# Optimization experiments

Measured on AMD Instinct MI355X. Metric: run time of the kernel, lower is better.

Reference implementation:

```python
import jax, jax.numpy as jnp
import numpy as np

L, CIN, CKV, E, H, D, NQ, NK = 3, 128, 256, 128, 8, 16, 4096, 1024
CLAMP_MAX = 65503.0  # torch.clamp(max=65503)
SCALE = 1.0 / (D * D)  # non-standard: 1 / projection_dim**2


def group_norm(x, w, b, groups, eps=1e-5):
    # x: [..., C, N]; w, b broadcastable to x.shape[:-1] (i.e. lead + (C,))
    lead = x.shape[:-2]
    C, N = x.shape[-2:]
    xg = x.reshape(lead + (groups, C // groups, N))
    mu = xg.mean(axis=(-2, -1), keepdims=True)
    var = ((xg - mu) ** 2).mean(axis=(-2, -1), keepdims=True)
    xn = ((xg - mu) * jax.lax.rsqrt(var + eps)).reshape(lead + (C, N))
    return xn * w[..., None] + b[..., None]


def split_heads(t):
    # [L, 1, E, N] -> [L, 1, H, N, D]
    l, b, e, n = t.shape
    return t.transpose(0, 1, 3, 2).reshape(l, b, n, H, D).transpose(0, 1, 3, 2, 4)


def setup_inputs():
    key = jax.random.key(0)
    ks = jax.random.split(key, 18)
    r = lambda k, s: jax.random.normal(k, s, dtype=jnp.float32)
    return {
        'x': r(ks[0], (1, CIN, NQ)),
        'x_global': r(ks[1], (L, CKV, NK)),
        'xyz': r(ks[2], (1, NQ, 3)),
        'xyz_global': r(ks[3], (L, NK, 3)),
        'gn1_w': r(ks[4], (CIN,)), 'gn1_b': r(ks[5], (CIN,)),
        'gn2_w': r(ks[6], (L, CKV)), 'gn2_b': r(ks[7], (L, CKV)),
        'qw': r(ks[8], (L, E, CIN)) * 0.05, 'qb': r(ks[9], (L, E)),
        'kw': r(ks[10], (L, E, CKV)) * 0.05, 'kb': r(ks[11], (L, E)),
        'vw': r(ks[12], (L, E, CKV)) * 0.05, 'vb': r(ks[13], (L, E)),
        'qgn_w': r(ks[14], (L, E)), 'qgn_b': r(ks[15], (L, E)),
        'cw': r(ks[16], (L, CIN, E)) * 0.05, 'cb': r(ks[17], (L, CIN)),
    }


def reference(x, x_global, xyz, xyz_global, gn1_w, gn1_b, gn2_w, gn2_b,
              qw, qb, kw, kb, vw, vb, qgn_w, qgn_b, cw, cb):
    # pre-norm of query features (shared across layers): [1, CIN, NQ]
    xq = jax.nn.relu(group_norm(x, gn1_w, gn1_b, 8))
    # per-source KV features: [L, 1, CKV, NK]
    xg = jax.nn.relu(group_norm(x_global[:, None], gn2_w[:, None], gn2_b[:, None], 16))

    # conv1d (kernel=1) projections + the shared q_gn GroupNorm(8, E)
    q = jnp.einsum('lec,bcn->lben', qw, xq) + qb[:, None, :, None]        # [L,1,E,NQ]
    q = group_norm(q, qgn_w[:, None], qgn_b[:, None], 8)
    k = jnp.einsum('lec,lbcn->lben', kw, xg) + kb[:, None, :, None]       # [L,1,E,NK]
    k = group_norm(k, qgn_w[:, None], qgn_b[:, None], 8)
    v = jnp.einsum('lec,lbcn->lben', vw, xg) + vb[:, None, :, None]       # [L,1,E,NK]
    v = group_norm(v, qgn_w[:, None], qgn_b[:, None], 8)

    qh, kh, vh = split_heads(q), split_heads(k), split_heads(v)           # [L,1,H,*,D]

    score = jnp.einsum('lbhqd,lbhkd->lbhqk', qh * SCALE, kh)              # [L,1,H,NQ,NK]
    score = jnp.minimum(score, CLAMP_MAX)
    w_att = jax.nn.softmax(score, axis=-1)
    o = jnp.einsum('lbhqk,lbhkd->lbhqd', w_att, vh)                        # [L,1,H,NQ,D]
    o = o.transpose(0, 1, 3, 2, 4).reshape(L, 1, NQ, E)                    # merge heads
    o = jnp.einsum('lbqe,loe->lbqo', o, cw) + cb[:, None, None, :]         # combine heads
    o = o.transpose(0, 1, 3, 2) + xq[None]                                 # [L,1,CIN,NQ], SA residual

    out = o.mean(axis=0) + x                                               # mean over sources + block residual
    return out, w_att[-1]                                                  # weight of last layer, as in torch loop
```

## Files before the change

### kernel.cpp

```cpp
#include <hip/hip_runtime.h>
#include <math.h>

constexpr int NQ = 4096, NK = 1024, CIN = 128, CKV = 256, E = 128, H = 8, D = 16, LAYERS = 3;
constexpr float SCALE = 1.0f / 256.0f;
constexpr float LOG2E = 1.44269504088896340736f;

typedef __bf16 bf16x8 __attribute__((ext_vector_type(8)));
typedef __bf16 bf16x4 __attribute__((ext_vector_type(4)));
typedef float f32x16 __attribute__((ext_vector_type(16)));
typedef float f32x4 __attribute__((ext_vector_type(4)));

__device__ __forceinline__ float exp2_fast(float x) {
#if __has_builtin(__builtin_amdgcn_exp2f)
  return __builtin_amdgcn_exp2f(x);
#else
  return exp2f(x);
#endif
}

__device__ __forceinline__ float rcp_fast(float x) {
#if __has_builtin(__builtin_amdgcn_rcpf)
  return __builtin_amdgcn_rcpf(x);
#else
  return 1.f / x;
#endif
}

__device__ __forceinline__ void block_reduce2(float& a, float& b, float* red) {
#pragma unroll
  for (int off = 32; off > 0; off >>= 1) {
    a += __shfl_down(a, off, 64);
    b += __shfl_down(b, off, 64);
  }
  int lane = threadIdx.x & 63, wid = threadIdx.x >> 6;
  if (lane == 0) { red[wid * 2] = a; red[wid * 2 + 1] = b; }
  __syncthreads();
  if (threadIdx.x == 0) {
    float sa = 0.f, sb = 0.f;
#pragma unroll
    for (int w = 0; w < 4; w++) { sa += red[w * 2]; sb += red[w * 2 + 1]; }
    red[0] = sa; red[1] = sb;
  }
  __syncthreads();
  a = red[0]; b = red[1];
}

__global__ __launch_bounds__(256) void pre_partial(const float* __restrict__ x,
                                                   const float* __restrict__ xg,
                                                   const float* __restrict__ qw,
                                                   const float* __restrict__ kw,
                                                   const float* __restrict__ vw,
                                                   float* __restrict__ acc,
                                                   __bf16* __restrict__ qwb,
                                                   __bf16* __restrict__ kwb,
                                                   __bf16* __restrict__ vwb) {
  int b = blockIdx.x, t = threadIdx.x;
  if (b >= 640) {
    int i = b - 640;
    const float* src; __bf16* dst; int off;
    if (i < 24)      { src = qw; dst = qwb; off = i * 2048; }
    else if (i < 72) { src = kw; dst = kwb; off = (i - 24) * 2048; }
    else             { src = vw; dst = vwb; off = (i - 72) * 2048; }
    int base = off + t * 8;
    float4 a = *(const float4*)(src + base);
    float4 c = *(const float4*)(src + base + 4);
    bf16x8 o = { (__bf16)a.x, (__bf16)a.y, (__bf16)a.z, (__bf16)a.w,
                 (__bf16)c.x, (__bf16)c.y, (__bf16)c.z, (__bf16)c.w };
    *(bf16x8*)(dst + base) = o;
    return;
  }
  __shared__ float red[8];
  const float4* p;
  int aidx;
  if (b < 256) { p = (const float4*)x + (size_t)b * 512; aidx = b >> 5; }
  else { int i = b - 256; p = (const float4*)xg + (size_t)i * 512; aidx = 8 + (i >> 3); }
  float s = 0.f, sq = 0.f;
#pragma unroll
  for (int i = 0; i < 2; i++) {
    float4 v = p[t + i * 256];
    s += v.x + v.y + v.z + v.w;
    sq += v.x * v.x + v.y * v.y + v.z * v.z + v.w * v.w;
  }
  block_reduce2(s, sq, red);
  if (t == 0) {
    atomicAdd(&acc[aidx * 2], s);
    atomicAdd(&acc[aidx * 2 + 1], sq);
  }
}

__global__ __launch_bounds__(256) void stage_a(const float* __restrict__ x,
                                               const float* __restrict__ xg,
                                               const float* __restrict__ acc,
                                               const float* __restrict__ gn1w,
                                               const float* __restrict__ gn1b,
                                               const float* __restrict__ gn2w,
                                               const float* __restrict__ gn2b,
                                               __bf16* __restrict__ xq_t,
                                               __bf16* __restrict__ xg_t) {
  int b = blockIdx.x, t = threadIdx.x;
  __shared__ float T[128 * 36];
  const float* in; __bf16* out; int N, Cout, ccbase, n0, gbase;
  const float* gw; const float* gb; float inv;
  if (b < 128) {
    in = x; N = NQ; out = xq_t; Cout = 128; ccbase = 0; n0 = b * 32;
    gw = gn1w; gb = gn1b; gbase = 0; inv = 1.f / 65536.f;
  } else {
    int i = b - 128; int l = i / 64; int r = i % 64; int ch = r >> 5;
    n0 = (r & 31) * 32;
    in = xg + ((size_t)l * 256 + ch * 128) * 1024; N = NK;
    out = xg_t + (size_t)l * 1024 * 256; Cout = 256; ccbase = ch * 128;
    gw = gn2w + l * 256 + ch * 128; gb = gn2b + l * 256 + ch * 128;
    gbase = 8 + l * 16 + ch * 8; inv = 1.f / 16384.f;
  }
  int nq = t & 7, cbase = t >> 3;
#pragma unroll
  for (int i = 0; i < 4; i++) {
    int c = cbase + 32 * i;
    int g = gbase + (c >> 4);
    float mu = acc[2 * g] * inv;
    float rs = rsqrtf(acc[2 * g + 1] * inv - mu * mu + 1e-5f);
    float sc = gw[c] * rs, sh = gb[c] - mu * sc;
    float4 v = *(const float4*)(in + (size_t)c * N + n0 + nq * 4);
    float4 o;
    o.x = fmaxf(v.x * sc + sh, 0.f);
    o.y = fmaxf(v.y * sc + sh, 0.f);
    o.z = fmaxf(v.z * sc + sh, 0.f);
    o.w = fmaxf(v.w * sc + sh, 0.f);
    *(float4*)(T + c * 36 + nq * 4) = o;
  }
  __syncthreads();
  int n = t >> 3, c0 = (t & 7) * 16;
  bf16x8 o1, o2;
#pragma unroll
  for (int j = 0; j < 8; j++) {
    o1[j] = (__bf16)T[(c0 + j) * 36 + n];
    o2[j] = (__bf16)T[(c0 + 8 + j) * 36 + n];
  }
  __bf16* op = out + (size_t)(n0 + n) * Cout + ccbase + c0;
  *(bf16x8*)op = o1;
  *(bf16x8*)(op + 8) = o2;
}

template <int KSTEPS>
__device__ __forceinline__ void gemm_tile(const __bf16* __restrict__ A,
                                          const __bf16* __restrict__ Bm,
                                          int stride, f32x16& acc, int l31, int half) {
#pragma unroll
  for (int ks = 0; ks < KSTEPS; ks++) {
    bf16x8 af = *(const bf16x8*)(A + (size_t)l31 * stride + ks * 16 + half * 8);
    bf16x8 bf = *(const bf16x8*)(Bm + (size_t)l31 * stride + ks * 16 + half * 8);
    acc = __builtin_amdgcn_mfma_f32_32x32x16_bf16(af, bf, acc, 0, 0, 0);
  }
}

__global__ __launch_bounds__(256) void proj_mfma(const __bf16* __restrict__ xq_t,
                                                 const __bf16* __restrict__ xg_t,
                                                 const __bf16* __restrict__ qwb,
                                                 const __bf16* __restrict__ kwb,
                                                 const __bf16* __restrict__ vwb,
                                                 const float* __restrict__ qb,
                                                 const float* __restrict__ kb,
                                                 const float* __restrict__ vb,
                                                 __bf16* __restrict__ q_raw,
                                                 __bf16* __restrict__ k_raw,
                                                 __bf16* __restrict__ v_raw,
                                                 float* __restrict__ qgnAcc) {
  int t = threadIdx.x;
  int w = blockIdx.x * 4 + (t >> 6);
  int lane = t & 63, l31 = lane & 31, half = lane >> 5;
  f32x16 acc = {0.f,0.f,0.f,0.f,0.f,0.f,0.f,0.f,0.f,0.f,0.f,0.f,0.f,0.f,0.f,0.f};
  int mat, l, e0, n0, N;
  const __bf16* A; const __bf16* Bm; const float* bias;
  if (w < 1536) {
    mat = 0; l = w >> 9; int r = w & 511; e0 = (r & 3) * 32; n0 = (r >> 2) * 32;
    N = NQ; A = qwb + (size_t)l * 128 * 128; Bm = xq_t; bias = qb + l * 128;
  } else if (w < 1920) {
    mat = 1; int idx = w - 1536; l = idx >> 7; int r = idx & 127;
    e0 = (r & 3) * 32; n0 = (r >> 2) * 32;
    N = NK; A = kwb + (size_t)l * 128 * 256; Bm = xg_t + (size_t)l * 1024 * 256;
    bias = kb + l * 128;
  } else {
    mat = 2; int idx = w - 1920; l = idx >> 7; int r = idx & 127;
    e0 = (r & 3) * 32; n0 = (r >> 2) * 32;
    N = NK; A = vwb + (size_t)l * 128 * 256; Bm = xg_t + (size_t)l * 1024 * 256;
    bias = vb + l * 128;
  }
  if (mat == 0) {
    gemm_tile<8>(A + (size_t)e0 * 128, Bm + (size_t)n0 * 128, 128, acc, l31, half);
  } else {
    gemm_tile<16>(A + (size_t)e0 * 256, Bm + (size_t)n0 * 256, 256, acc, l31, half);
  }

  float vals[16];
  float s0 = 0.f, sq0 = 0.f, s1 = 0.f, sq1 = 0.f;
#pragma unroll
  for (int r = 0; r < 16; r++) {
    int row = (r & 3) + 8 * (r >> 2) + 4 * half;
    float v = acc[r] + bias[e0 + row];
    vals[r] = v;
    if (r < 8) { s0 += v; sq0 += v * v; } else { s1 += v; sq1 += v * v; }
  }
#pragma unroll
  for (int off = 1; off < 64; off <<= 1) {
    s0 += __shfl_xor(s0, off); sq0 += __shfl_xor(sq0, off);
    s1 += __shfl_xor(s1, off); sq1 += __shfl_xor(sq1, off);
  }
  int gbase = (mat == 0 ? 0 : (mat == 1 ? 24 : 48)) + l * 8 + (e0 >> 4);
  if (lane == 0) {
    atomicAdd(&qgnAcc[gbase * 2], s0);
    atomicAdd(&qgnAcc[gbase * 2 + 1], sq0);
    atomicAdd(&qgnAcc[(gbase + 1) * 2], s1);
    atomicAdd(&qgnAcc[(gbase + 1) * 2 + 1], sq1);
  }
  if (mat < 2) {
    __bf16* out = (mat == 0 ? q_raw : k_raw);
#pragma unroll
    for (int qd = 0; qd < 4; qd++) {
      int h = (e0 >> 4) + (qd >> 1);
      int d0 = 4 * half + 8 * (qd & 1);
      bf16x4 o;
#pragma unroll
      for (int j = 0; j < 4; j++) o[j] = (__bf16)vals[qd * 4 + j];
      *(bf16x4*)(out + ((size_t)(l * 8 + h) * N + n0 + l31) * 16 + d0) = o;
    }
  } else {
#pragma unroll
    for (int r = 0; r < 16; r++) {
      int row = (r & 3) + 8 * (r >> 2) + 4 * half;
      int h = (e0 >> 4) + (row >> 4);
      v_raw[((size_t)(l * 8 + h) * 16 + (row & 15)) * NK + n0 + l31] = (__bf16)vals[r];
    }
  }
}

__global__ __launch_bounds__(256) void attn_kernel(const __bf16* __restrict__ qbf,
                                                   const __bf16* __restrict__ kbf,
                                                   const __bf16* __restrict__ vbf,
                                                   const float* __restrict__ qgnAcc,
                                                   const float* __restrict__ qgnw,
                                                   const float* __restrict__ qgnb,
                                                   float* __restrict__ ob,
                                                   float* __restrict__ rinv_ws) {
  __shared__ __bf16 Pt[4][32 * 40];

  const int t = threadIdx.x;
  const int wv = t >> 6;
  const int lane = t & 63;
  const int l31 = lane & 31, half = lane >> 5, l15 = lane & 15, quad = lane >> 4;
  const int h = blockIdx.y, l = blockIdx.z;
  const int q0 = blockIdx.x * 128 + wv * 32;

  const __bf16* Qh = qbf + (size_t)(l * H + h) * NQ * D;
  const __bf16* Kh = kbf + (size_t)(l * H + h) * NK * D;
  const __bf16* Vh = vbf + (size_t)(l * H + h) * D * NK;

  const int gq = l * 8 + h, gk = 24 + l * 8 + h, gv = 48 + l * 8 + h;
  const float invq = 1.f / 65536.f, invkv = 1.f / 16384.f;
  const float muq = qgnAcc[2 * gq] * invq;
  const float rsq = rsqrtf(qgnAcc[2 * gq + 1] * invq - muq * muq + 1e-5f);
  const float muk = qgnAcc[2 * gk] * invkv;
  const float rsk = rsqrtf(qgnAcc[2 * gk + 1] * invkv - muk * muk + 1e-5f);
  const float muv = qgnAcc[2 * gv] * invkv;
  const float rsv = rsqrtf(qgnAcc[2 * gv + 1] * invkv - muv * muv + 1e-5f);

  const int cbase = l * 128 + h * 16;
  bf16x8 qfrag;
  {
    const float EX = SCALE * LOG2E;
    bf16x8 qraw = *(const bf16x8*)(Qh + (size_t)(q0 + l31) * D + half * 8);
#pragma unroll
    for (int j = 0; j < 8; j++) {
      float w = qgnw[cbase + half * 8 + j], bb = qgnb[cbase + half * 8 + j];
      float wq = w * rsq;
      float qe = (float)qraw[j] * (wq * EX) + (bb - muq * wq) * EX;
      qfrag[j] = (__bf16)(qe * (w * rsk));
    }
  }
  const float va = qgnw[cbase + l15] * rsv;
  const float vc = qgnb[cbase + l15] - muv * va;

  bf16x8 ones;
#pragma unroll
  for (int j = 0; j < 8; j++) ones[j] = (__bf16)1.0f;

  f32x4 oa0 = {0.f, 0.f, 0.f, 0.f}, oa1 = {0.f, 0.f, 0.f, 0.f};
  f32x4 sa0 = {0.f, 0.f, 0.f, 0.f}, sa1 = {0.f, 0.f, 0.f, 0.f};

  __bf16* Pw = &Pt[wv][0];

  for (int c = 0; c < 32; ++c) {
    const int k0 = c * 32;
    bf16x8 kf = *(const bf16x8*)(Kh + (size_t)(k0 + l31) * D + half * 8);
    f32x16 s = {0.f,0.f,0.f,0.f,0.f,0.f,0.f,0.f,0.f,0.f,0.f,0.f,0.f,0.f,0.f,0.f};
    s = __builtin_amdgcn_mfma_f32_32x32x16_bf16(qfrag, kf, s, 0, 0, 0);
#pragma unroll
    for (int r = 0; r < 16; ++r) {
      float p = exp2_fast(s[r]);
      int row = (r & 3) + 8 * (r >> 2) + 4 * half;
      Pw[row * 40 + l31] = (__bf16)p;
    }
    bf16x8 a0 = *(const bf16x8*)(Pw + l15 * 40 + quad * 8);
    bf16x8 a1 = *(const bf16x8*)(Pw + (16 + l15) * 40 + quad * 8);
    bf16x8 bv = *(const bf16x8*)(Vh + (size_t)l15 * NK + k0 + quad * 8);
    oa0 = __builtin_amdgcn_mfma_f32_16x16x32_bf16(a0, bv, oa0, 0, 0, 0);
    oa1 = __builtin_amdgcn_mfma_f32_16x16x32_bf16(a1, bv, oa1, 0, 0, 0);
    sa0 = __builtin_amdgcn_mfma_f32_16x16x32_bf16(a0, ones, sa0, 0, 0, 0);
    sa1 = __builtin_amdgcn_mfma_f32_16x16x32_bf16(a1, ones, sa1, 0, 0, 0);
  }

  if (l == 2 && l15 == 0) {
#pragma unroll
    for (int r = 0; r < 4; ++r) {
      rinv_ws[(size_t)h * NQ + q0 + quad * 4 + r] = rcp_fast(sa0[r]);
      rinv_ws[(size_t)h * NQ + q0 + 16 + quad * 4 + r] = rcp_fast(sa1[r]);
    }
  }

  float* Ow = (float*)Pw;
#pragma unroll
  for (int r = 0; r < 4; ++r) {
    int qa = quad * 4 + r;
    Ow[l15 * 36 + qa] = oa0[r] * rcp_fast(sa0[r]) * va + vc;
    Ow[l15 * 36 + 16 + qa] = oa1[r] * rcp_fast(sa1[r]) * va + vc;
  }
  {
    int dd = lane >> 2, j = (lane & 3) * 8;
    float4 u0 = *(const float4*)(Ow + dd * 36 + j);
    float4 u1 = *(const float4*)(Ow + dd * 36 + j + 4);
    size_t rb = (size_t)(l * E + h * D + dd) * NQ + q0 + j;
    *(float4*)(ob + rb) = u0;
    *(float4*)(ob + rb + 4) = u1;
  }
}

__global__ __launch_bounds__(256) void post_kernel(const __bf16* __restrict__ qbf,
                                                   const __bf16* __restrict__ kbf,
                                                   const float* __restrict__ rinv_ws,
                                                   const float* __restrict__ qgnAcc,
                                                   const float* __restrict__ qgnw,
                                                   const float* __restrict__ qgnb,
                                                   const float* __restrict__ x,
                                                   const float* __restrict__ accAll,
                                                   const float* __restrict__ gn1w,
                                                   const float* __restrict__ gn1b,
                                                   const float* __restrict__ ob,
                                                   const float* __restrict__ cw,
                                                   const float* __restrict__ cb,
                                                   float* __restrict__ out,
                                                   float* __restrict__ wout) {
  __shared__ float S[128 * 16];
  const int blk = blockIdx.x, t = threadIdx.x;
  if (blk < 512) {
    const int wv = t >> 6, lane = t & 63;
    const int l31 = lane & 31, half = lane >> 5;
    const int qtile = blk & 31, h = (blk >> 5) & 7, khalf = blk >> 8;
    const int q0 = qtile * 128 + wv * 32;
    const int kbase = khalf * 512;

    const __bf16* Qh = qbf + (size_t)(2 * H + h) * NQ * D;
    const __bf16* Kh = kbf + (size_t)(2 * H + h) * NK * D;

    const int gq = 16 + h, gk = 24 + 16 + h;
    const float invq = 1.f / 65536.f, invkv = 1.f / 16384.f;
    const float muq = qgnAcc[2 * gq] * invq;
    const float rsq = rsqrtf(qgnAcc[2 * gq + 1] * invq - muq * muq + 1e-5f);
    const float muk = qgnAcc[2 * gk] * invkv;
    const float rsk = rsqrtf(qgnAcc[2 * gk + 1] * invkv - muk * muk + 1e-5f);

    const int cbase = 2 * 128 + h * 16;
    bf16x8 qfrag;
    {
      const float EX = SCALE * LOG2E;
      bf16x8 qraw = *(const bf16x8*)(Qh + (size_t)(q0 + l31) * D + half * 8);
#pragma unroll
      for (int j = 0; j < 8; j++) {
        float w = qgnw[cbase + half * 8 + j], bb = qgnb[cbase + half * 8 + j];
        float wq = w * rsq;
        float qe = (float)qraw[j] * (wq * EX) + (bb - muq * wq) * EX;
        qfrag[j] = (__bf16)(qe * (w * rsk));
      }
    }

    float riv[16];
#pragma unroll
    for (int r = 0; r < 16; ++r)
      riv[r] = rinv_ws[(size_t)h * NQ + q0 + (r & 3) + 8 * (r >> 2) + 4 * half];

    for (int c = 0; c < 16; ++c) {
      const int k0 = kbase + c * 32;
      bf16x8 kf = *(const bf16x8*)(Kh + (size_t)(k0 + l31) * D + half * 8);
      f32x16 s = {0.f,0.f,0.f,0.f,0.f,0.f,0.f,0.f,0.f,0.f,0.f,0.f,0.f,0.f,0.f,0.f};
      s = __builtin_amdgcn_mfma_f32_32x32x16_bf16(qfrag, kf, s, 0, 0, 0);
#pragma unroll
      for (int r = 0; r < 16; ++r) {
        float p = exp2_fast(s[r]) * riv[r];
        int row = (r & 3) + 8 * (r >> 2) + 4 * half;
        __builtin_nontemporal_store(p, &wout[(size_t)(h * NQ + q0 + row) * NK + k0 + l31]);
      }
    }
    return;
  }

  const int nt0 = (blk - 512) * 16;
  const int c0 = (t >> 2) * 2;
  const int nf = t & 3;
  float4 a0 = make_float4(0.f, 0.f, 0.f, 0.f);
  float4 a1 = make_float4(0.f, 0.f, 0.f, 0.f);
  for (int l = 0; l < LAYERS; l++) {
    if (l) __syncthreads();
#pragma unroll
    for (int i = 0; i < 2; i++) {
      int fid = i * 256 + t;
      int e = fid >> 2, pos = fid & 3;
      *(float4*)(S + e * 16 + pos * 4) =
          *(const float4*)(ob + ((size_t)l * E + e) * NQ + nt0 + pos * 4);
    }
    __syncthreads();
    const float* cwl = cw + (size_t)l * CIN * E;
#pragma unroll 8
    for (int e4 = 0; e4 < E / 4; e4++) {
      const int e = e4 * 4;
      float4 w0 = *(const float4*)(cwl + (size_t)c0 * E + e);
      float4 w1 = *(const float4*)(cwl + (size_t)(c0 + 1) * E + e);
      float4 s0 = *(const float4*)(S + (e + 0) * 16 + nf * 4);
      float4 s1 = *(const float4*)(S + (e + 1) * 16 + nf * 4);
      float4 s2 = *(const float4*)(S + (e + 2) * 16 + nf * 4);
      float4 s3 = *(const float4*)(S + (e + 3) * 16 + nf * 4);
      a0.x += w0.x * s0.x + w0.y * s1.x + w0.z * s2.x + w0.w * s3.x;
      a0.y += w0.x * s0.y + w0.y * s1.y + w0.z * s2.y + w0.w * s3.y;
      a0.z += w0.x * s0.z + w0.y * s1.z + w0.z * s2.z + w0.w * s3.z;
      a0.w += w0.x * s0.w + w0.y * s1.w + w0.z * s2.w + w0.w * s3.w;
      a1.x += w1.x * s0.x + w1.y * s1.x + w1.z * s2.x + w1.w * s3.x;
      a1.y += w1.x * s0.y + w1.y * s1.y + w1.z * s2.y + w1.w * s3.y;
      a1.z += w1.x * s0.z + w1.y * s1.z + w1.z * s2.z + w1.w * s3.z;
      a1.w += w1.x * s0.w + w1.y * s1.w + w1.z * s2.w + w1.w * s3.w;
    }
  }
  const float third = 1.f / 3.f;
#pragma unroll
  for (int i = 0; i < 2; i++) {
    int c = c0 + i;
    float4 a = i ? a1 : a0;
    float bsum = (cb[c] + cb[CIN + c] + cb[2 * CIN + c]) * third;
    int g = c >> 4;
    const float inv = 1.f / 65536.f;
    float mu = accAll[2 * g] * inv;
    float rs = rsqrtf(accAll[2 * g + 1] * inv - mu * mu + 1e-5f);
    float sc = gn1w[c] * rs, sh = gn1b[c] - mu * sc;
    size_t off = (size_t)c * NQ + nt0 + nf * 4;
    float4 xv = *(const float4*)(x + off);
    float4 o;
    o.x = xv.x + fmaxf(xv.x * sc + sh, 0.f) + a.x * third + bsum;
    o.y = xv.y + fmaxf(xv.y * sc + sh, 0.f) + a.y * third + bsum;
    o.z = xv.z + fmaxf(xv.z * sc + sh, 0.f) + a.z * third + bsum;
    o.w = xv.w + fmaxf(xv.w * sc + sh, 0.f) + a.w * third + bsum;
    *(float4*)(out + off) = o;
  }
}

extern "C" void kernel_launch(void* const* d_in, const int* in_sizes, int n_in,
                              void* d_out, int out_size, void* d_ws, size_t ws_size,
                              hipStream_t stream) {
  (void)in_sizes; (void)n_in; (void)out_size;
  const float* x    = (const float*)d_in[0];
  const float* xgi  = (const float*)d_in[1];
  const float* gn1w = (const float*)d_in[4];
  const float* gn1b = (const float*)d_in[5];
  const float* gn2w = (const float*)d_in[6];
  const float* gn2b = (const float*)d_in[7];
  const float* qw   = (const float*)d_in[8];
  const float* qb   = (const float*)d_in[9];
  const float* kw   = (const float*)d_in[10];
  const float* kb   = (const float*)d_in[11];
  const float* vw   = (const float*)d_in[12];
  const float* vb   = (const float*)d_in[13];
  const float* qgnw = (const float*)d_in[14];
  const float* qgnb = (const float*)d_in[15];
  const float* cw   = (const float*)d_in[16];
  const float* cb   = (const float*)d_in[17];

  float* ws = (float*)d_ws;
  __bf16* xq_t  = (__bf16*)ws;
  __bf16* xg_t  = (__bf16*)(ws + 262144);
  __bf16* qwb   = (__bf16*)(ws + 655360);
  __bf16* kwb   = (__bf16*)(ws + 679936);
  __bf16* vwb   = (__bf16*)(ws + 729088);
  __bf16* q_raw = (__bf16*)(ws + 778240);
  __bf16* k_raw = (__bf16*)(ws + 1564672);
  __bf16* v_raw = (__bf16*)(ws + 1761280);
  float*  ob    = ws + 1957888;
  float*  accAll = ws + 3530752;
  float*  rinv_ws = ws + 3531008;
  if (ws_size < (size_t)3563776 * sizeof(float)) return;

  float* qgnAcc = accAll + 112;
  float* outp = (float*)d_out;
  float* wout = outp + 524288;

  hipMemsetAsync(accAll, 0, 256 * sizeof(float), stream);

  pre_partial<<<760, 256, 0, stream>>>(x, xgi, qw, kw, vw, accAll, qwb, kwb, vwb);

  stage_a<<<320, 256, 0, stream>>>(x, xgi, accAll, gn1w, gn1b, gn2w, gn2b, xq_t, xg_t);

  proj_mfma<<<576, 256, 0, stream>>>(xq_t, xg_t, qwb, kwb, vwb, qb, kb, vb,
                                     q_raw, k_raw, v_raw, qgnAcc);

  attn_kernel<<<dim3(32, 8, 3), 256, 0, stream>>>(q_raw, k_raw, v_raw,
                                                  qgnAcc, qgnw, qgnb, ob, rinv_ws);

  post_kernel<<<768, 256, 0, stream>>>(q_raw, k_raw, rinv_ws, qgnAcc, qgnw, qgnb,
                                       x, accAll, gn1w, gn1b, ob, cw, cb, outp, wout);
}
```

Before: 276.1 us.

## Keep attention probabilities in registers via transposed MFMA and permlane swaps

```diff
diff --git a/kernel.cpp b/kernel.cpp
--- a/kernel.cpp
+++ b/kernel.cpp
@@ -7,8 +7,10 @@
 
 typedef __bf16 bf16x8 __attribute__((ext_vector_type(8)));
 typedef __bf16 bf16x4 __attribute__((ext_vector_type(4)));
+typedef __bf16 bf16x2 __attribute__((ext_vector_type(2)));
 typedef float f32x16 __attribute__((ext_vector_type(16)));
 typedef float f32x4 __attribute__((ext_vector_type(4)));
+typedef unsigned u32x4 __attribute__((ext_vector_type(4)));
 
 __device__ __forceinline__ float exp2_fast(float x) {
 #if __has_builtin(__builtin_amdgcn_exp2f)
@@ -23,6 +25,20 @@
   return __builtin_amdgcn_rcpf(x);
 #else
   return 1.f / x;
+#endif
+}
+
+__device__ __forceinline__ void swap32(unsigned a, unsigned b, unsigned& o1, unsigned& o2) {
+#if __has_builtin(__builtin_amdgcn_permlane32_swap)
+  auto r = __builtin_amdgcn_permlane32_swap((int)a, (int)b, false, false);
+  o1 = (unsigned)r[0];
+  o2 = (unsigned)r[1];
+#else
+  unsigned ax = (unsigned)__shfl_xor((int)a, 32, 64);
+  unsigned bx = (unsigned)__shfl_xor((int)b, 32, 64);
+  bool hi = (threadIdx.x & 32) != 0;
+  o1 = hi ? bx : a;
+  o2 = hi ? b : ax;
 #endif
 }
 
@@ -241,12 +257,10 @@
                                                    const float* __restrict__ qgnb,
                                                    float* __restrict__ ob,
                                                    float* __restrict__ rinv_ws) {
-  __shared__ __bf16 Pt[4][32 * 40];
-
   const int t = threadIdx.x;
   const int wv = t >> 6;
   const int lane = t & 63;
-  const int l31 = lane & 31, half = lane >> 5, l15 = lane & 15, quad = lane >> 4;
+  const int l31 = lane & 31, half = lane >> 5;
   const int h = blockIdx.y, l = blockIdx.z;
   const int q0 = blockIdx.x * 128 + wv * 32;
 
@@ -276,60 +290,55 @@
       qfrag[j] = (__bf16)(qe * (w * rsk));
     }
   }
-  const float va = qgnw[cbase + l15] * rsv;
-  const float vc = qgnb[cbase + l15] - muv * va;
-
-  bf16x8 ones;
-#pragma unroll
-  for (int j = 0; j < 8; j++) ones[j] = (__bf16)1.0f;
-
-  f32x4 oa0 = {0.f, 0.f, 0.f, 0.f}, oa1 = {0.f, 0.f, 0.f, 0.f};
-  f32x4 sa0 = {0.f, 0.f, 0.f, 0.f}, sa1 = {0.f, 0.f, 0.f, 0.f};
-
-  __bf16* Pw = &Pt[wv][0];
+
+  const int dvrow = l31 & 15;
+
+  f32x16 oacc = {0.f,0.f,0.f,0.f,0.f,0.f,0.f,0.f,0.f,0.f,0.f,0.f,0.f,0.f,0.f,0.f};
+  float rsum = 0.f;
 
   for (int c = 0; c < 32; ++c) {
     const int k0 = c * 32;
     bf16x8 kf = *(const bf16x8*)(Kh + (size_t)(k0 + l31) * D + half * 8);
     f32x16 s = {0.f,0.f,0.f,0.f,0.f,0.f,0.f,0.f,0.f,0.f,0.f,0.f,0.f,0.f,0.f,0.f};
-    s = __builtin_amdgcn_mfma_f32_32x32x16_bf16(qfrag, kf, s, 0, 0, 0);
-#pragma unroll
-    for (int r = 0; r < 16; ++r) {
-      float p = exp2_fast(s[r]);
-      int row = (r & 3) + 8 * (r >> 2) + 4 * half;
-      Pw[row * 40 + l31] = (__bf16)p;
-    }
-    bf16x8 a0 = *(const bf16x8*)(Pw + l15 * 40 + quad * 8);
-    bf16x8 a1 = *(const bf16x8*)(Pw + (16 + l15) * 40 + quad * 8);
-    bf16x8 bv = *(const bf16x8*)(Vh + (size_t)l15 * NK + k0 + quad * 8);
-    oa0 = __builtin_amdgcn_mfma_f32_16x16x32_bf16(a0, bv, oa0, 0, 0, 0);
-    oa1 = __builtin_amdgcn_mfma_f32_16x16x32_bf16(a1, bv, oa1, 0, 0, 0);
-    sa0 = __builtin_amdgcn_mfma_f32_16x16x32_bf16(a0, ones, sa0, 0, 0, 0);
-    sa1 = __builtin_amdgcn_mfma_f32_16x16x32_bf16(a1, ones, sa1, 0, 0, 0);
-  }
-
-  if (l == 2 && l15 == 0) {
-#pragma unroll
-    for (int r = 0; r < 4; ++r) {
-      rinv_ws[(size_t)h * NQ + q0 + quad * 4 + r] = rcp_fast(sa0[r]);
-      rinv_ws[(size_t)h * NQ + q0 + 16 + quad * 4 + r] = rcp_fast(sa1[r]);
-    }
-  }
-
-  float* Ow = (float*)Pw;
-#pragma unroll
-  for (int r = 0; r < 4; ++r) {
-    int qa = quad * 4 + r;
-    Ow[l15 * 36 + qa] = oa0[r] * rcp_fast(sa0[r]) * va + vc;
-    Ow[l15 * 36 + 16 + qa] = oa1[r] * rcp_fast(sa1[r]) * va + vc;
-  }
-  {
-    int dd = lane >> 2, j = (lane & 3) * 8;
-    float4 u0 = *(const float4*)(Ow + dd * 36 + j);
-    float4 u1 = *(const float4*)(Ow + dd * 36 + j + 4);
-    size_t rb = (size_t)(l * E + h * D + dd) * NQ + q0 + j;
-    *(float4*)(ob + rb) = u0;
-    *(float4*)(ob + rb + 4) = u1;
+    s = __builtin_amdgcn_mfma_f32_32x32x16_bf16(kf, qfrag, s, 0, 0, 0);
+    unsigned w[8];
+#pragma unroll
+    for (int j = 0; j < 8; ++j) {
+      float p0 = exp2_fast(s[2 * j]);
+      float p1 = exp2_fast(s[2 * j + 1]);
+      rsum += p0 + p1;
+      bf16x2 pk;
+      pk[0] = (__bf16)p0;
+      pk[1] = (__bf16)p1;
+      w[j] = __builtin_bit_cast(unsigned, pk);
+    }
+    unsigned b10, b11, b12, b13, b20, b21, b22, b23;
+    swap32(w[0], w[2], b10, b12);
+    swap32(w[1], w[3], b11, b13);
+    swap32(w[4], w[6], b20, b22);
+    swap32(w[5], w[7], b21, b23);
+    u32x4 u1 = {b10, b11, b12, b13};
+    u32x4 u2 = {b20, b21, b22, b23};
+    bf16x8 P1 = __builtin_bit_cast(bf16x8, u1);
+    bf16x8 P2 = __builtin_bit_cast(bf16x8, u2);
+    bf16x8 v1 = *(const bf16x8*)(Vh + (size_t)dvrow * NK + k0 + half * 8);
+    bf16x8 v2 = *(const bf16x8*)(Vh + (size_t)dvrow * NK + k0 + 16 + half * 8);
+    oacc = __builtin_amdgcn_mfma_f32_32x32x16_bf16(v1, P1, oacc, 0, 0, 0);
+    oacc = __builtin_amdgcn_mfma_f32_32x32x16_bf16(v2, P2, oacc, 0, 0, 0);
+  }
+
+  rsum += __shfl_xor(rsum, 32);
+  const float rinv = rcp_fast(rsum);
+
+  if (l == 2 && half == 0)
+    rinv_ws[(size_t)h * NQ + q0 + l31] = rinv;
+
+#pragma unroll
+  for (int r = 0; r < 8; ++r) {
+    int d = (r & 3) + 8 * (r >> 2) + 4 * half;
+    float va = qgnw[cbase + d] * rsv;
+    float vc = qgnb[cbase + d] - muv * va;
+    ob[(size_t)(l * E + h * D + d) * NQ + q0 + l31] = oacc[r] * rinv * va + vc;
   }
 }
 
```

Result: slower. 282.8 us (+2.4%).
